# Optimization experiments

Measured on AMD Instinct MI355X. Metric: run time of the kernel, lower is better.

## Reference

```python
import jax, jax.numpy as jnp
import numpy as np

EPS = 1e-7  # tf.keras.backend.epsilon()
ROUTING_ITERS = 3


def squash(v, axis=-1):
    s2 = jnp.sum(jnp.square(v), axis=axis, keepdims=True)
    scale = s2 / (1.0 + s2)
    return scale * v / jnp.sqrt(s2 + EPS)


def setup_inputs() -> dict:
    key = jax.random.key(0)
    k1, k2 = jax.random.split(key)
    B, N, IC, ID, OD = 64, 10, 6912, 16, 16
    x = jax.random.normal(k1, (B, IC, ID), dtype=jnp.float32)
    # glorot-uniform-ish scale for W [N, IC, ID, OD]
    limit = np.sqrt(6.0 / (ID + OD)).astype(np.float32)
    W = jax.random.uniform(k2, (N, IC, ID, OD), dtype=jnp.float32, minval=-limit, maxval=limit)
    return {"x": x, "W": W}


def reference(x, W):
    # x: [B, IC, ID]; W: [N, IC, ID, OD]
    # inputs_hat[b,n,j,o] = sum_i x[b,j,i] * W[n,j,i,o]
    u_hat = jnp.einsum('bji,njio->bnjo', x, W)  # [B, N, IC, OD]
    B, N, IC, _ = u_hat.shape
    b = jnp.zeros((B, N, IC), dtype=u_hat.dtype)
    v = None
    for i in range(ROUTING_ITERS):
        c = jax.nn.softmax(b, axis=1)                    # [B, N, IC]
        s = jnp.einsum('bnj,bnjo->bno', c, u_hat)        # [B, N, OD]
        v = squash(s)                                     # [B, N, OD]
        if i < ROUTING_ITERS - 1:
            b = b + jnp.einsum('bnjo,bno->bnj', u_hat, v)
    return v
```

## Files before the change

### kernel.cpp

```cpp
#include <hip/hip_runtime.h>
#include <math.h>

#define NCAP 10
#define IC   6912
#define NJG  576
#define NSLOT (NJG * 2)
#define JPG  12
#define WPAIRS ((IC * NCAP) / 2)

typedef __attribute__((ext_vector_type(4))) float f32x4;
typedef __attribute__((ext_vector_type(8))) short bf16x8;

static __device__ inline unsigned short f2bf(float f) {
    unsigned int u = __float_as_uint(f);
    unsigned int r = u + 0x7FFFu + ((u >> 16) & 1u);
    return (unsigned short)(r >> 16);
}

__global__ __launch_bounds__(256) void prep_kernel(
    const float* __restrict__ x, const float* __restrict__ W,
    unsigned short* __restrict__ w_t, unsigned short* __restrict__ x_t,
    int use_xt)
{
    __shared__ float lds[4 * 1312];
    const int tid  = threadIdx.x;
    const int lane = tid & 63;
    const int wv   = tid >> 6;

    if (blockIdx.x < 1024) {
        float* L0 = lds + wv * 1312;
        const int gw = blockIdx.x * 4 + wv;
        const int lr  = lane & 31;
        const int reg = lane >> 5;
        const int ia  = lr >> 2, oq = lr & 3;
        const int o   = lr & 15, kq2 = lr >> 4;
        const float4* W4 = (const float4*)W;
        int itc = 0;
        for (int p = gw; p < WPAIRS; p += 4096, ++itc) {
            float* L = L0 + (itc & 1) * 656;
            const int tl = p * 2 + reg;
            const int n = tl % 10, j = tl / 10;
            const float4* src = W4 + ((size_t)n * IC + j) * 64;
            float4 a = src[lr];
            float4 c = src[lr + 32];
            *(float4*)&L[reg * 328 + ia * 20 + oq * 4] = a;
            *(float4*)&L[reg * 328 + (ia + 8) * 20 + oq * 4] = c;
            bf16x8 fr;
            #pragma unroll
            for (int t = 0; t < 8; ++t)
                fr[t] = (short)f2bf(L[reg * 328 + (kq2 * 8 + t) * 20 + o]);
            *(bf16x8*)&w_t[(size_t)tl * 256 + lr * 8] = fr;
        }
    } else if (use_xt) {
        const int j  = blockIdx.x - 1024;
        const int bg = wv;
        if (lane < 32) {
            const int bl = lane & 15, kq = lane >> 4;
            const float* xp = x + ((size_t)(bg * 16 + bl) * IC + j) * 16 + kq * 8;
            float4 x0 = *(const float4*)xp;
            float4 x1 = *(const float4*)(xp + 4);
            bf16x8 fr;
            fr[0] = (short)f2bf(x0.x); fr[1] = (short)f2bf(x0.y);
            fr[2] = (short)f2bf(x0.z); fr[3] = (short)f2bf(x0.w);
            fr[4] = (short)f2bf(x1.x); fr[5] = (short)f2bf(x1.y);
            fr[6] = (short)f2bf(x1.z); fr[7] = (short)f2bf(x1.w);
            *(bf16x8*)&x_t[((size_t)j * 4 + bg) * 256 + lane * 8] = fr;
        }
    }
}

__global__ __launch_bounds__(256, 4) void sweep_kernel(
    const float* __restrict__ x, const unsigned short* __restrict__ x_t,
    const unsigned short* __restrict__ w_t, const float* __restrict__ vsum,
    float* __restrict__ part, int iter, int use_xt)
{
    __shared__ float smem[32 * 164 + 128];

    const int tid  = threadIdx.x;
    const int lane = tid & 63;
    const int wave = tid >> 6;
    const int bl   = lane & 15;
    const int kq   = lane >> 4;
    const bool act = (lane < 32);
    const int logical = ((int)blockIdx.x & 7) * (NSLOT / 8) + ((int)blockIdx.x >> 3);
    const int bh   = logical & 1;
    const int jg   = logical >> 1;
    const int bg_l = wave & 1;
    const int nh   = wave >> 1;
    const int b    = bh * 32 + bg_l * 16 + bl;
    const int j0   = jg * JPG;
    const int vrow = (bg_l * 16 + bl) * 164;
    float* exbuf = smem + 5248;

    const f32x4 zf = (f32x4){0.f, 0.f, 0.f, 0.f};
    const bf16x8 zb = (bf16x8){0, 0, 0, 0, 0, 0, 0, 0};

    if (iter > 0) {
        const float4* vs4 = (const float4*)(vsum + bh * 5120);
        for (int i = tid; i < 1280; i += 256) {
            const int row = i / 40, col = (i % 40) * 4;
            *(float4*)&smem[row * 164 + col] = vs4[i];
        }
    }
    __syncthreads();

    f32x4 sac[5];
    #pragma unroll
    for (int p = 0; p < 5; ++p) sac[p] = zf;

    bf16x8 fw[5]; bf16x8 fx;
    fx = zb;
    #pragma unroll
    for (int p = 0; p < 5; ++p) fw[p] = zb;
    if (act) {
        if (use_xt) {
            fx = *(const bf16x8*)&x_t[((size_t)j0 * 4 + bh * 2 + bg_l) * 256 + lane * 8];
        } else {
            const float* xp = x + ((size_t)b * IC + j0) * 16 + kq * 8;
            float4 x0 = *(const float4*)xp, x1 = *(const float4*)(xp + 4);
            fx[0] = (short)f2bf(x0.x); fx[1] = (short)f2bf(x0.y);
            fx[2] = (short)f2bf(x0.z); fx[3] = (short)f2bf(x0.w);
            fx[4] = (short)f2bf(x1.x); fx[5] = (short)f2bf(x1.y);
            fx[6] = (short)f2bf(x1.z); fx[7] = (short)f2bf(x1.w);
        }
        #pragma unroll
        for (int p = 0; p < 5; ++p)
            fw[p] = *(const bf16x8*)&w_t[((size_t)j0 * NCAP + nh * 5 + p) * 256 + lane * 8];
    }

    #pragma unroll
    for (int jt = 0; jt < JPG; ++jt) {
        const int j1 = j0 + jt + 1;

        bf16x8 nx = zb;
        if (jt < JPG - 1 && act) {
            if (use_xt) {
                nx = *(const bf16x8*)&x_t[((size_t)j1 * 4 + bh * 2 + bg_l) * 256 + lane * 8];
            } else {
                const float* xp = x + ((size_t)b * IC + j1) * 16 + kq * 8;
                float4 x0 = *(const float4*)xp, x1 = *(const float4*)(xp + 4);
                nx[0] = (short)f2bf(x0.x); nx[1] = (short)f2bf(x0.y);
                nx[2] = (short)f2bf(x0.z); nx[3] = (short)f2bf(x0.w);
                nx[4] = (short)f2bf(x1.x); nx[5] = (short)f2bf(x1.y);
                nx[6] = (short)f2bf(x1.z); nx[7] = (short)f2bf(x1.w);
            }
        }

        f32x4 u[5];
        #pragma unroll
        for (int p = 0; p < 5; ++p)
            u[p] = __builtin_amdgcn_mfma_f32_16x16x32_bf16(fw[p], fx, zf, 0, 0, 0);

        if (jt < JPG - 1 && act) {
            #pragma unroll
            for (int p = 0; p < 5; ++p)
                fw[p] = *(const bf16x8*)&w_t[((size_t)j1 * NCAP + nh * 5 + p) * 256 + lane * 8];
        }

        if (iter == 0) {
            #pragma unroll
            for (int p = 0; p < 5; ++p) {
                sac[p][0] = fmaf(0.1f, u[p][0], sac[p][0]);
                sac[p][1] = fmaf(0.1f, u[p][1], sac[p][1]);
                sac[p][2] = fmaf(0.1f, u[p][2], sac[p][2]);
                sac[p][3] = fmaf(0.1f, u[p][3], sac[p][3]);
            }
        } else {
            float cc[5];
            #pragma unroll
            for (int p = 0; p < 5; ++p) {
                f32x4 vvn = *(const f32x4*)&smem[vrow + (nh * 5 + p) * 16 + kq * 4];
                float pr = u[p][0] * vvn[0] + u[p][1] * vvn[1]
                         + u[p][2] * vvn[2] + u[p][3] * vvn[3];
                pr += __shfl_xor(pr, 16);
                pr += __shfl_xor(pr, 32);
                cc[p] = pr;
            }
            float s5 = 0.f;
            #pragma unroll
            for (int p = 0; p < 5; ++p) { cc[p] = __expf(cc[p]); s5 += cc[p]; }
            float* ex = exbuf + (jt & 1) * 64;
            if (kq == 0) ex[nh * 32 + bg_l * 16 + bl] = s5;
            __syncthreads();
            const float so = ex[(1 - nh) * 32 + bg_l * 16 + bl];
            const float inv = 1.0f / (s5 + so);
            #pragma unroll
            for (int p = 0; p < 5; ++p) {
                const float cn = cc[p] * inv;
                sac[p][0] = fmaf(cn, u[p][0], sac[p][0]);
                sac[p][1] = fmaf(cn, u[p][1], sac[p][1]);
                sac[p][2] = fmaf(cn, u[p][2], sac[p][2]);
                sac[p][3] = fmaf(cn, u[p][3], sac[p][3]);
            }
        }

        fx = nx;
    }

    float* pp = part + (size_t)logical * 5120;
    #pragma unroll
    for (int p = 0; p < 5; ++p)
        *(f32x4*)&pp[(bg_l * 16 + bl) * 160 + (nh * 5 + p) * 16 + kq * 4] = sac[p];
}

__global__ __launch_bounds__(1024) void reduce_kernel(
    const float* __restrict__ part, float* __restrict__ vsum,
    float* __restrict__ out, int iter)
{
    __shared__ float lds[15 * 64];
    const int tid = threadIdx.x;
    const int gi = tid & 63, rq = tid >> 6;
    const int g  = blockIdx.x * 64 + gi;
    const float* p0 = part + g;
    float acc = 0.f;
    for (int k = rq * 36; k < rq * 36 + 36; ++k)
        acc += p0[(size_t)k * 10240];
    if (rq > 0) lds[(rq - 1) * 64 + gi] = acc;
    __syncthreads();
    if (rq == 0) {
        #pragma unroll
        for (int r = 0; r < 15; ++r) acc += lds[r * 64 + gi];
        float sq = acc * acc;
        sq += __shfl_xor(sq, 1);
        sq += __shfl_xor(sq, 2);
        sq += __shfl_xor(sq, 4);
        sq += __shfl_xor(sq, 8);
        float scale = (sq / (1.f + sq)) / sqrtf(sq + 1e-7f);
        float v = scale * acc;
        if (iter == 2)      out[g] = v;
        else if (iter == 0) vsum[g] = v;
        else                vsum[g] += v;
    }
}

extern "C" void kernel_launch(void* const* d_in, const int* in_sizes, int n_in,
                              void* d_out, int out_size, void* d_ws, size_t ws_size,
                              hipStream_t stream) {
    (void)in_sizes; (void)n_in; (void)out_size;
    const float* x = (const float*)d_in[0];
    const float* W = (const float*)d_in[1];
    float* out = (float*)d_out;

    const size_t wt_sh = (size_t)IC * NCAP * 256;
    const size_t xt_sh = (size_t)IC * 4 * 256;
    const size_t part_f = (size_t)NSLOT * 5120;
    const size_t need_xt = wt_sh * 2 + xt_sh * 2 + part_f * 4 + 10240 * 4;

    int use_xt = (ws_size >= need_xt) ? 1 : 0;
    unsigned short* w_t = (unsigned short*)d_ws;
    unsigned short* x_t = use_xt ? (w_t + wt_sh) : nullptr;
    float* part = (float*)(use_xt ? (void*)(x_t + xt_sh) : (void*)(w_t + wt_sh));
    float* vsum = part + part_f;

    prep_kernel<<<use_xt ? (1024 + IC) : 1024, 256, 0, stream>>>(x, W, w_t, x_t, use_xt);
    for (int iter = 0; iter < 3; ++iter) {
        sweep_kernel<<<NSLOT, 256, 0, stream>>>(x, x_t, w_t, vsum, part, iter, use_xt);
        reduce_kernel<<<160, 1024, 0, stream>>>(part, vsum, out, iter);
    }
}
```

Measured before the change: 219.9 us.

## Fuse W/x bf16 conversion into first routing sweep, drop prep kernel

Removes the separate prep kernel and has iteration 0 of the sweep kernel load fp32 W and x directly, transpose them through LDS, convert to bf16, and use them right away in the MFMAs. The converted tiles are also written to the workspace for the later iterations. This saves one launch and a full extra pass over W. In exchange, the first sweep does more work per block: W is loaded redundantly by both batch halves (only bh==0 writes it back), and the pair-wise shuffle handling for the odd capsule count adds complexity.

```diff
diff --git a/kernel.cpp b/kernel.cpp
--- a/kernel.cpp
+++ b/kernel.cpp
@@ -6,7 +6,6 @@
 #define NJG  576
 #define NSLOT (NJG * 2)
 #define JPG  12
-#define WPAIRS ((IC * NCAP) / 2)
 
 typedef __attribute__((ext_vector_type(4))) float f32x4;
 typedef __attribute__((ext_vector_type(8))) short bf16x8;
@@ -17,62 +16,19 @@
     return (unsigned short)(r >> 16);
 }
 
-__global__ __launch_bounds__(256) void prep_kernel(
+static __device__ inline bf16x8 shfl32(bf16x8 v) {
+    union { bf16x8 s; int i[4]; } u;
+    u.s = v;
+    #pragma unroll
+    for (int t = 0; t < 4; ++t) u.i[t] = __shfl_xor(u.i[t], 32);
+    return u.s;
+}
+
+__global__ __launch_bounds__(256, 4) void sweep_kernel(
     const float* __restrict__ x, const float* __restrict__ W,
-    unsigned short* __restrict__ w_t, unsigned short* __restrict__ x_t,
-    int use_xt)
-{
-    __shared__ float lds[4 * 1312];
-    const int tid  = threadIdx.x;
-    const int lane = tid & 63;
-    const int wv   = tid >> 6;
-
-    if (blockIdx.x < 1024) {
-        float* L0 = lds + wv * 1312;
-        const int gw = blockIdx.x * 4 + wv;
-        const int lr  = lane & 31;
-        const int reg = lane >> 5;
-        const int ia  = lr >> 2, oq = lr & 3;
-        const int o   = lr & 15, kq2 = lr >> 4;
-        const float4* W4 = (const float4*)W;
-        int itc = 0;
-        for (int p = gw; p < WPAIRS; p += 4096, ++itc) {
-            float* L = L0 + (itc & 1) * 656;
-            const int tl = p * 2 + reg;
-            const int n = tl % 10, j = tl / 10;
-            const float4* src = W4 + ((size_t)n * IC + j) * 64;
-            float4 a = src[lr];
-            float4 c = src[lr + 32];
-            *(float4*)&L[reg * 328 + ia * 20 + oq * 4] = a;
-            *(float4*)&L[reg * 328 + (ia + 8) * 20 + oq * 4] = c;
-            bf16x8 fr;
-            #pragma unroll
-            for (int t = 0; t < 8; ++t)
-                fr[t] = (short)f2bf(L[reg * 328 + (kq2 * 8 + t) * 20 + o]);
-            *(bf16x8*)&w_t[(size_t)tl * 256 + lr * 8] = fr;
-        }
-    } else if (use_xt) {
-        const int j  = blockIdx.x - 1024;
-        const int bg = wv;
-        if (lane < 32) {
-            const int bl = lane & 15, kq = lane >> 4;
-            const float* xp = x + ((size_t)(bg * 16 + bl) * IC + j) * 16 + kq * 8;
-            float4 x0 = *(const float4*)xp;
-            float4 x1 = *(const float4*)(xp + 4);
-            bf16x8 fr;
-            fr[0] = (short)f2bf(x0.x); fr[1] = (short)f2bf(x0.y);
-            fr[2] = (short)f2bf(x0.z); fr[3] = (short)f2bf(x0.w);
-            fr[4] = (short)f2bf(x1.x); fr[5] = (short)f2bf(x1.y);
-            fr[6] = (short)f2bf(x1.z); fr[7] = (short)f2bf(x1.w);
-            *(bf16x8*)&x_t[((size_t)j * 4 + bg) * 256 + lane * 8] = fr;
-        }
-    }
-}
-
-__global__ __launch_bounds__(256, 4) void sweep_kernel(
-    const float* __restrict__ x, const unsigned short* __restrict__ x_t,
-    const unsigned short* __restrict__ w_t, const float* __restrict__ vsum,
-    float* __restrict__ part, int iter, int use_xt)
+    unsigned short* __restrict__ x_t, unsigned short* __restrict__ w_t,
+    const float* __restrict__ vsum, float* __restrict__ part,
+    int iter, int use_xt)
 {
     __shared__ float smem[32 * 164 + 128];
 
@@ -95,77 +51,129 @@
     const f32x4 zf = (f32x4){0.f, 0.f, 0.f, 0.f};
     const bf16x8 zb = (bf16x8){0, 0, 0, 0, 0, 0, 0, 0};
 
-    if (iter > 0) {
+    f32x4 sac[5];
+    #pragma unroll
+    for (int p = 0; p < 5; ++p) sac[p] = zf;
+
+    if (iter == 0) {
+        const int lr  = lane & 31;
+        const int reg = lane >> 5;
+        const int ia  = lr >> 2, oq = lr & 3;
+        const int o   = lr & 15, kq2 = lr >> 4;
+        float* L0 = smem + wave * 1312;
+        const float4* W4 = (const float4*)W;
+        const int nbase = nh * 5;
+
+        #pragma unroll
+        for (int jt = 0; jt < JPG; ++jt) {
+            const int j = j0 + jt;
+
+            bf16x8 fx = zb;
+            if (act) {
+                const float* xp = x + ((size_t)b * IC + j) * 16 + kq * 8;
+                float4 x0 = *(const float4*)xp, x1 = *(const float4*)(xp + 4);
+                fx[0] = (short)f2bf(x0.x); fx[1] = (short)f2bf(x0.y);
+                fx[2] = (short)f2bf(x0.z); fx[3] = (short)f2bf(x0.w);
+                fx[4] = (short)f2bf(x1.x); fx[5] = (short)f2bf(x1.y);
+                fx[6] = (short)f2bf(x1.z); fx[7] = (short)f2bf(x1.w);
+                if (use_xt && nh == 0)
+                    *(bf16x8*)&x_t[((size_t)j * 4 + bh * 2 + bg_l) * 256 + lane * 8] = fx;
+            }
+
+            bf16x8 fw[5];
+            #pragma unroll
+            for (int p = 0; p < 5; ++p) fw[p] = zb;
+            #pragma unroll
+            for (int pr = 0; pr < 3; ++pr) {
+                const int nA  = nbase + pr * 2;
+                const int nB  = (pr < 2) ? (nA + 1) : nA;
+                const int myn = reg ? nB : nA;
+                const int tl  = j * 10 + myn;
+                float* L = L0 + (pr & 1) * 656;
+                const float4* src = W4 + ((size_t)myn * IC + j) * 64;
+                float4 a = src[lr];
+                float4 c = src[lr + 32];
+                *(float4*)&L[reg * 328 + ia * 20 + oq * 4] = a;
+                *(float4*)&L[reg * 328 + (ia + 8) * 20 + oq * 4] = c;
+                bf16x8 fr;
+                #pragma unroll
+                for (int t = 0; t < 8; ++t)
+                    fr[t] = (short)f2bf(L[reg * 328 + (kq2 * 8 + t) * 20 + o]);
+                if (bh == 0)
+                    *(bf16x8*)&w_t[(size_t)tl * 256 + lr * 8] = fr;
+                bf16x8 fo = shfl32(fr);
+                if (act) {
+                    fw[pr * 2] = fr;
+                    if (pr < 2) fw[pr * 2 + 1] = fo;
+                }
+            }
+
+            #pragma unroll
+            for (int p = 0; p < 5; ++p) {
+                f32x4 u = __builtin_amdgcn_mfma_f32_16x16x32_bf16(fw[p], fx, zf, 0, 0, 0);
+                sac[p][0] = fmaf(0.1f, u[0], sac[p][0]);
+                sac[p][1] = fmaf(0.1f, u[1], sac[p][1]);
+                sac[p][2] = fmaf(0.1f, u[2], sac[p][2]);
+                sac[p][3] = fmaf(0.1f, u[3], sac[p][3]);
+            }
+        }
+    } else {
         const float4* vs4 = (const float4*)(vsum + bh * 5120);
         for (int i = tid; i < 1280; i += 256) {
             const int row = i / 40, col = (i % 40) * 4;
             *(float4*)&smem[row * 164 + col] = vs4[i];
         }
-    }
-    __syncthreads();
-
-    f32x4 sac[5];
-    #pragma unroll
-    for (int p = 0; p < 5; ++p) sac[p] = zf;
-
-    bf16x8 fw[5]; bf16x8 fx;
-    fx = zb;
-    #pragma unroll
-    for (int p = 0; p < 5; ++p) fw[p] = zb;
-    if (act) {
-        if (use_xt) {
-            fx = *(const bf16x8*)&x_t[((size_t)j0 * 4 + bh * 2 + bg_l) * 256 + lane * 8];
-        } else {
-            const float* xp = x + ((size_t)b * IC + j0) * 16 + kq * 8;
-            float4 x0 = *(const float4*)xp, x1 = *(const float4*)(xp + 4);
-            fx[0] = (short)f2bf(x0.x); fx[1] = (short)f2bf(x0.y);
-            fx[2] = (short)f2bf(x0.z); fx[3] = (short)f2bf(x0.w);
-            fx[4] = (short)f2bf(x1.x); fx[5] = (short)f2bf(x1.y);
-            fx[6] = (short)f2bf(x1.z); fx[7] = (short)f2bf(x1.w);
-        }
-        #pragma unroll
-        for (int p = 0; p < 5; ++p)
-            fw[p] = *(const bf16x8*)&w_t[((size_t)j0 * NCAP + nh * 5 + p) * 256 + lane * 8];
-    }
-
-    #pragma unroll
-    for (int jt = 0; jt < JPG; ++jt) {
-        const int j1 = j0 + jt + 1;
-
-        bf16x8 nx = zb;
-        if (jt < JPG - 1 && act) {
+        __syncthreads();
+
+        bf16x8 fw[5]; bf16x8 fx;
+        fx = zb;
+        #pragma unroll
+        for (int p = 0; p < 5; ++p) fw[p] = zb;
+        if (act) {
             if (use_xt) {
-                nx = *(const bf16x8*)&x_t[((size_t)j1 * 4 + bh * 2 + bg_l) * 256 + lane * 8];
+                fx = *(const bf16x8*)&x_t[((size_t)j0 * 4 + bh * 2 + bg_l) * 256 + lane * 8];
             } else {
-                const float* xp = x + ((size_t)b * IC + j1) * 16 + kq * 8;
+                const float* xp = x + ((size_t)b * IC + j0) * 16 + kq * 8;
                 float4 x0 = *(const float4*)xp, x1 = *(const float4*)(xp + 4);
-                nx[0] = (short)f2bf(x0.x); nx[1] = (short)f2bf(x0.y);
-                nx[2] = (short)f2bf(x0.z); nx[3] = (short)f2bf(x0.w);
-                nx[4] = (short)f2bf(x1.x); nx[5] = (short)f2bf(x1.y);
-                nx[6] = (short)f2bf(x1.z); nx[7] = (short)f2bf(x1.w);
-            }
-        }
-
-        f32x4 u[5];
-        #pragma unroll
-        for (int p = 0; p < 5; ++p)
-            u[p] = __builtin_amdgcn_mfma_f32_16x16x32_bf16(fw[p], fx, zf, 0, 0, 0);
-
-        if (jt < JPG - 1 && act) {
+                fx[0] = (short)f2bf(x0.x); fx[1] = (short)f2bf(x0.y);
+                fx[2] = (short)f2bf(x0.z); fx[3] = (short)f2bf(x0.w);
+                fx[4] = (short)f2bf(x1.x); fx[5] = (short)f2bf(x1.y);
+                fx[6] = (short)f2bf(x1.z); fx[7] = (short)f2bf(x1.w);
+            }
             #pragma unroll
             for (int p = 0; p < 5; ++p)
-                fw[p] = *(const bf16x8*)&w_t[((size_t)j1 * NCAP + nh * 5 + p) * 256 + lane * 8];
-        }
-
-        if (iter == 0) {
-            #pragma unroll
-            for (int p = 0; p < 5; ++p) {
-                sac[p][0] = fmaf(0.1f, u[p][0], sac[p][0]);
-                sac[p][1] = fmaf(0.1f, u[p][1], sac[p][1]);
-                sac[p][2] = fmaf(0.1f, u[p][2], sac[p][2]);
-                sac[p][3] = fmaf(0.1f, u[p][3], sac[p][3]);
-            }
-        } else {
+                fw[p] = *(const bf16x8*)&w_t[((size_t)j0 * NCAP + nh * 5 + p) * 256 + lane * 8];
+        }
+
+        #pragma unroll
+        for (int jt = 0; jt < JPG; ++jt) {
+            const int j1 = j0 + jt + 1;
+
+            bf16x8 nx = zb;
+            if (jt < JPG - 1 && act) {
+                if (use_xt) {
+                    nx = *(const bf16x8*)&x_t[((size_t)j1 * 4 + bh * 2 + bg_l) * 256 + lane * 8];
+                } else {
+                    const float* xp = x + ((size_t)b * IC + j1) * 16 + kq * 8;
+                    float4 x0 = *(const float4*)xp, x1 = *(const float4*)(xp + 4);
+                    nx[0] = (short)f2bf(x0.x); nx[1] = (short)f2bf(x0.y);
+                    nx[2] = (short)f2bf(x0.z); nx[3] = (short)f2bf(x0.w);
+                    nx[4] = (short)f2bf(x1.x); nx[5] = (short)f2bf(x1.y);
+                    nx[6] = (short)f2bf(x1.z); nx[7] = (short)f2bf(x1.w);
+                }
+            }
+
+            f32x4 u[5];
+            #pragma unroll
+            for (int p = 0; p < 5; ++p)
+                u[p] = __builtin_amdgcn_mfma_f32_16x16x32_bf16(fw[p], fx, zf, 0, 0, 0);
+
+            if (jt < JPG - 1 && act) {
+                #pragma unroll
+                for (int p = 0; p < 5; ++p)
+                    fw[p] = *(const bf16x8*)&w_t[((size_t)j1 * NCAP + nh * 5 + p) * 256 + lane * 8];
+            }
+
             float cc[5];
             #pragma unroll
             for (int p = 0; p < 5; ++p) {
@@ -192,9 +200,9 @@
                 sac[p][2] = fmaf(cn, u[p][2], sac[p][2]);
                 sac[p][3] = fmaf(cn, u[p][3], sac[p][3]);
             }
-        }
-
-        fx = nx;
+
+            fx = nx;
+        }
     }
 
     float* pp = part + (size_t)logical * 5120;
@@ -252,9 +260,8 @@
     float* part = (float*)(use_xt ? (void*)(x_t + xt_sh) : (void*)(w_t + wt_sh));
     float* vsum = part + part_f;
 
-    prep_kernel<<<use_xt ? (1024 + IC) : 1024, 256, 0, stream>>>(x, W, w_t, x_t, use_xt);
     for (int iter = 0; iter < 3; ++iter) {
-        sweep_kernel<<<NSLOT, 256, 0, stream>>>(x, x_t, w_t, vsum, part, iter, use_xt);
+        sweep_kernel<<<NSLOT, 256, 0, stream>>>(x, W, x_t, w_t, vsum, part, iter, use_xt);
         reduce_kernel<<<160, 1024, 0, stream>>>(part, vsum, out, iter);
     }
 }
```

Measured after the change: 658.6 us. 200% more time.
